# Optimization experiments

Hardware: AMD Instinct MI355X
Metric: run time of the kernel (lower is better)

## Reference

```python
import jax, jax.numpy as jnp
import numpy as np

BN_EPS = 1e-5
N_NODES = 131072
C_IN = 32
C_OUT = 32
K = 27  # 3x3x3 kernel taps


def setup_inputs() -> dict:
    key = jax.random.key(0)
    k1, k2, k3 = jax.random.split(key, 3)
    data_in = jax.random.normal(k1, (1, C_IN, N_NODES, 1), dtype=jnp.float32)
    neigh = jax.random.randint(k2, (N_NODES, K), 0, N_NODES, dtype=jnp.int32)
    weight = jax.random.normal(k3, (K * C_IN, C_OUT), dtype=jnp.float32) * (1.0 / np.sqrt(K * C_IN))
    gamma = jnp.ones((C_OUT,), dtype=jnp.float32)
    beta = jnp.zeros((C_OUT,), dtype=jnp.float32)
    return {"data_in": data_in, "neigh": neigh, "weight": weight, "gamma": gamma, "beta": beta}


def reference(data_in, neigh, weight, gamma, beta):
    # data_in: [1, C_in, N, 1] -> node-major features [N, C_in]
    x = jnp.transpose(data_in[0, :, :, 0])  # [N, C_in]
    # Octree sparse conv: gather 27-neighborhood per node, then matmul.
    g = x[neigh]                              # [N, K, C_in] irregular gather
    g = g.reshape(g.shape[0], K * C_IN)       # [N, K*C_in]
    out = g @ weight                          # [N, C_out]
    # BatchNorm2d over [1, C_out, N, 1]: per-channel stats over the N nodes (training mode, biased var)
    mean = jnp.mean(out, axis=0)
    var = jnp.mean(jnp.square(out - mean), axis=0)
    out = (out - mean) * jax.lax.rsqrt(var + BN_EPS) * gamma + beta
    # ReLU
    out = jnp.maximum(out, 0.0)
    # back to O-CNN layout [1, C_out, N, 1]
    return jnp.transpose(out)[None, :, :, None]
```

## Files before the change

### kernel.cpp

```cpp
#include <hip/hip_runtime.h>

#define N_NODES 131072
#define C_IN 32
#define C_OUT 32
#define KTAPS 27
#define BN_EPS 1e-5f
#define NPASS 3

typedef __bf16 bf16x8 __attribute__((ext_vector_type(8)));
typedef float  f32x4  __attribute__((ext_vector_type(4)));


static __device__ __forceinline__ unsigned short f2bf(float f) {
    unsigned int u = __float_as_uint(f);
    unsigned int r = (u + 0x7FFFu + ((u >> 16) & 1u)) >> 16;
    return (unsigned short)r;
}

__global__ __launch_bounds__(256) void k_prep(const float* __restrict__ in,
                                              const float* __restrict__ w,
                                              unsigned short* __restrict__ xb,
                                              unsigned short* __restrict__ wlay,
                                              float* __restrict__ sums) {
    if (blockIdx.x < N_NODES / 256) {
        const int n = blockIdx.x * 256 + threadIdx.x;
        unsigned short v[C_IN];
#pragma unroll
        for (int c = 0; c < C_IN; ++c) v[c] = f2bf(in[(size_t)c * N_NODES + n]);
        uint4* dst = reinterpret_cast<uint4*>(xb + (size_t)n * C_IN);
#pragma unroll
        for (int q = 0; q < 4; ++q) {
            uint4 pk;
            pk.x = (unsigned)v[q * 8 + 0] | ((unsigned)v[q * 8 + 1] << 16);
            pk.y = (unsigned)v[q * 8 + 2] | ((unsigned)v[q * 8 + 3] << 16);
            pk.z = (unsigned)v[q * 8 + 4] | ((unsigned)v[q * 8 + 5] << 16);
            pk.w = (unsigned)v[q * 8 + 6] | ((unsigned)v[q * 8 + 7] << 16);
            dst[q] = pk;
        }
    } else {
        if (threadIdx.x < 4) {
            uint4 z = {0u, 0u, 0u, 0u};
            reinterpret_cast<uint4*>(xb + (size_t)N_NODES * C_IN)[threadIdx.x] = z;
        }
        if (threadIdx.x < 2 * C_OUT) sums[threadIdx.x] = 0.f;
        for (int g = threadIdx.x; g < KTAPS * 2 * 64; g += 256) {
            const int k = g >> 7;
            const int rem = g & 127;
            const int h = rem >> 6;
            const int l = rem & 63;
            unsigned short wv[8];
#pragma unroll
            for (int j = 0; j < 8; ++j) {
                const int c  = ((l >> 4) << 3) + j;
                const int co = (h << 4) + (l & 15);
                wv[j] = f2bf(w[(size_t)(k * C_IN + c) * C_OUT + co]);
            }
            uint4 pk;
            pk.x = (unsigned)wv[0] | ((unsigned)wv[1] << 16);
            pk.y = (unsigned)wv[2] | ((unsigned)wv[3] << 16);
            pk.z = (unsigned)wv[4] | ((unsigned)wv[5] << 16);
            pk.w = (unsigned)wv[6] | ((unsigned)wv[7] << 16);
            *reinterpret_cast<uint4*>(wlay + (size_t)g * 8) = pk;
        }
    }
}

__global__ __launch_bounds__(1024) void k_conv_mfma(const unsigned short* __restrict__ xb,
                                                    const int* __restrict__ neigh,
                                                    const unsigned short* __restrict__ wlay,
                                                    float* __restrict__ out,
                                                    float* __restrict__ sums) {
    __shared__ unsigned short wl[KTAPS * 2 * 64 * 8];
    __shared__ float bs[C_OUT];
    __shared__ float bq[C_OUT];

    {
        const uint4* src = reinterpret_cast<const uint4*>(wlay);
        uint4* d = reinterpret_cast<uint4*>(wl);
        for (int i = threadIdx.x; i < KTAPS * 2 * 64; i += 1024) d[i] = src[i];
    }
    if (threadIdx.x < C_OUT) { bs[threadIdx.x] = 0.f; bq[threadIdx.x] = 0.f; }
    __syncthreads();

    const int wid  = threadIdx.x >> 6;
    const int lane = threadIdx.x & 63;
    const int lr   = lane & 15;
    const int lg   = lane >> 4;
    const int nb   = blockIdx.x * 256 + wid * 16;

    const int* nrow = neigh + (size_t)(nb + lr) * KTAPS;
    int nidx[KTAPS];
#pragma unroll
    for (int k = 0; k < KTAPS; ++k) nidx[k] = nrow[k];

    f32x4 acc0 = {0.f, 0.f, 0.f, 0.f};
    f32x4 acc1 = {0.f, 0.f, 0.f, 0.f};

#pragma unroll 1
    for (int p = 0; p < NPASS; ++p) {
        const int lo = (p * N_NODES) / NPASS;
        const int hi = ((p + 1) * N_NODES) / NPASS;
#pragma unroll
        for (int k = 0; k < KTAPS; ++k) {
            const int idx = nidx[k];
            const int src = (idx >= lo) && (idx < hi) ? idx : N_NODES;
            const bf16x8 xf = *reinterpret_cast<const bf16x8*>(xb + (size_t)src * C_IN + lg * 8);
            const bf16x8 w0 = *reinterpret_cast<const bf16x8*>(wl + ((size_t)(k * 2 + 0) * 64 + lane) * 8);
            const bf16x8 w1 = *reinterpret_cast<const bf16x8*>(wl + ((size_t)(k * 2 + 1) * 64 + lane) * 8);
            acc0 = __builtin_amdgcn_mfma_f32_16x16x32_bf16(w0, xf, acc0, 0, 0, 0);
            acc1 = __builtin_amdgcn_mfma_f32_16x16x32_bf16(w1, xf, acc1, 0, 0, 0);
        }
        __syncthreads();
    }

#pragma unroll
    for (int r = 0; r < 4; ++r) {
        out[(size_t)(lg * 4 + r) * N_NODES + nb + lr]      = acc0[r];
        out[(size_t)(16 + lg * 4 + r) * N_NODES + nb + lr] = acc1[r];
    }

    float s0[4], q0[4], s1[4], q1[4];
#pragma unroll
    for (int r = 0; r < 4; ++r) {
        s0[r] = acc0[r]; q0[r] = acc0[r] * acc0[r];
        s1[r] = acc1[r]; q1[r] = acc1[r] * acc1[r];
    }
#pragma unroll
    for (int off = 1; off < 16; off <<= 1) {
#pragma unroll
        for (int r = 0; r < 4; ++r) {
            s0[r] += __shfl_xor(s0[r], off); q0[r] += __shfl_xor(q0[r], off);
            s1[r] += __shfl_xor(s1[r], off); q1[r] += __shfl_xor(q1[r], off);
        }
    }
    if (lr == 0) {
#pragma unroll
        for (int r = 0; r < 4; ++r) {
            atomicAdd(&bs[lg * 4 + r], s0[r]);      atomicAdd(&bq[lg * 4 + r], q0[r]);
            atomicAdd(&bs[16 + lg * 4 + r], s1[r]); atomicAdd(&bq[16 + lg * 4 + r], q1[r]);
        }
    }
    __syncthreads();
    if (threadIdx.x < C_OUT) {
        atomicAdd(&sums[threadIdx.x], bs[threadIdx.x]);
        atomicAdd(&sums[C_OUT + threadIdx.x], bq[threadIdx.x]);
    }
}

__global__ __launch_bounds__(256) void k_bnrelu(float* __restrict__ out,
                                                const float* __restrict__ sums,
                                                const float* __restrict__ gamma,
                                                const float* __restrict__ beta) {
    const size_t gid = (size_t)blockIdx.x * 256 + threadIdx.x;
    const int co = (int)(gid / (N_NODES / 4));
    const float inv_n = 1.0f / (float)N_NODES;
    const float mean = sums[co] * inv_n;
    const float var  = sums[C_OUT + co] * inv_n - mean * mean;
    const float scale = rsqrtf(var + BN_EPS) * gamma[co];
    const float bias  = beta[co] - mean * scale;

    float4* p = reinterpret_cast<float4*>(out);
    float4 v = p[gid];
    v.x = fmaxf(fmaf(v.x, scale, bias), 0.0f);
    v.y = fmaxf(fmaf(v.y, scale, bias), 0.0f);
    v.z = fmaxf(fmaf(v.z, scale, bias), 0.0f);
    v.w = fmaxf(fmaf(v.w, scale, bias), 0.0f);
    p[gid] = v;
}

extern "C" void kernel_launch(void* const* d_in, const int* in_sizes, int n_in,
                              void* d_out, int out_size, void* d_ws, size_t ws_size,
                              hipStream_t stream) {
    const float* data_in = (const float*)d_in[0];
    const int*   neigh   = (const int*)d_in[1];
    const float* weight  = (const float*)d_in[2];
    const float* gamma   = (const float*)d_in[3];
    const float* beta    = (const float*)d_in[4];
    float* out = (float*)d_out;

    unsigned short* xb   = (unsigned short*)d_ws;
    unsigned short* wlay = xb + (size_t)(N_NODES + 1) * C_IN;
    float* sums = (float*)(wlay + (size_t)KTAPS * 2 * 64 * 8);

    k_prep<<<N_NODES / 256 + 1, 256, 0, stream>>>(data_in, weight, xb, wlay, sums);
    k_conv_mfma<<<N_NODES / 256, 1024, 0, stream>>>(xb, neigh, wlay, out, sums);
    k_bnrelu<<<(N_NODES * C_OUT / 4) / 256, 256, 0, stream>>>(out, sums, gamma, beta);
}
```

Measured before the change: 73.12 us.

## Switch conv to 32x32x16 MFMA with 32 nodes per wave

```diff
diff --git a/kernel.cpp b/kernel.cpp
--- a/kernel.cpp
+++ b/kernel.cpp
@@ -8,7 +8,7 @@
 #define NPASS 3
 
 typedef __bf16 bf16x8 __attribute__((ext_vector_type(8)));
-typedef float  f32x4  __attribute__((ext_vector_type(4)));
+typedef float  f32x16 __attribute__((ext_vector_type(16)));
 
 
 static __device__ __forceinline__ unsigned short f2bf(float f) {
@@ -45,14 +45,13 @@
         if (threadIdx.x < 2 * C_OUT) sums[threadIdx.x] = 0.f;
         for (int g = threadIdx.x; g < KTAPS * 2 * 64; g += 256) {
             const int k = g >> 7;
-            const int rem = g & 127;
-            const int h = rem >> 6;
-            const int l = rem & 63;
+            const int h = (g >> 6) & 1;
+            const int l = g & 63;
             unsigned short wv[8];
 #pragma unroll
             for (int j = 0; j < 8; ++j) {
-                const int c  = ((l >> 4) << 3) + j;
-                const int co = (h << 4) + (l & 15);
+                const int c  = h * 16 + ((l >> 5) << 3) + j;
+                const int co = l & 31;
                 wv[j] = f2bf(w[(size_t)(k * C_IN + c) * C_OUT + co]);
             }
             uint4 pk;
@@ -65,11 +64,11 @@
     }
 }
 
-__global__ __launch_bounds__(1024) void k_conv_mfma(const unsigned short* __restrict__ xb,
-                                                    const int* __restrict__ neigh,
-                                                    const unsigned short* __restrict__ wlay,
-                                                    float* __restrict__ out,
-                                                    float* __restrict__ sums) {
+__global__ __launch_bounds__(512, 4) void k_conv_mfma(const unsigned short* __restrict__ xb,
+                                                      const int* __restrict__ neigh,
+                                                      const unsigned short* __restrict__ wlay,
+                                                      float* __restrict__ out,
+                                                      float* __restrict__ sums) {
     __shared__ unsigned short wl[KTAPS * 2 * 64 * 8];
     __shared__ float bs[C_OUT];
     __shared__ float bq[C_OUT];
@@ -77,24 +76,23 @@
     {
         const uint4* src = reinterpret_cast<const uint4*>(wlay);
         uint4* d = reinterpret_cast<uint4*>(wl);
-        for (int i = threadIdx.x; i < KTAPS * 2 * 64; i += 1024) d[i] = src[i];
+        for (int i = threadIdx.x; i < KTAPS * 2 * 64; i += 512) d[i] = src[i];
     }
     if (threadIdx.x < C_OUT) { bs[threadIdx.x] = 0.f; bq[threadIdx.x] = 0.f; }
     __syncthreads();
 
     const int wid  = threadIdx.x >> 6;
     const int lane = threadIdx.x & 63;
-    const int lr   = lane & 15;
-    const int lg   = lane >> 4;
-    const int nb   = blockIdx.x * 256 + wid * 16;
+    const int col  = lane & 31;
+    const int kh   = lane >> 5;
+    const int nb   = blockIdx.x * 256 + wid * 32;
 
-    const int* nrow = neigh + (size_t)(nb + lr) * KTAPS;
+    const int* nrow = neigh + (size_t)(nb + col) * KTAPS;
     int nidx[KTAPS];
 #pragma unroll
     for (int k = 0; k < KTAPS; ++k) nidx[k] = nrow[k];
 
-    f32x4 acc0 = {0.f, 0.f, 0.f, 0.f};
-    f32x4 acc1 = {0.f, 0.f, 0.f, 0.f};
+    f32x16 acc = {};
 
 #pragma unroll 1
     for (int p = 0; p < NPASS; ++p) {
@@ -104,40 +102,40 @@
         for (int k = 0; k < KTAPS; ++k) {
             const int idx = nidx[k];
             const int src = (idx >= lo) && (idx < hi) ? idx : N_NODES;
-            const bf16x8 xf = *reinterpret_cast<const bf16x8*>(xb + (size_t)src * C_IN + lg * 8);
+            const unsigned short* xrow = xb + (size_t)src * C_IN + kh * 8;
+            const bf16x8 x0 = *reinterpret_cast<const bf16x8*>(xrow);
+            const bf16x8 x1 = *reinterpret_cast<const bf16x8*>(xrow + 16);
             const bf16x8 w0 = *reinterpret_cast<const bf16x8*>(wl + ((size_t)(k * 2 + 0) * 64 + lane) * 8);
             const bf16x8 w1 = *reinterpret_cast<const bf16x8*>(wl + ((size_t)(k * 2 + 1) * 64 + lane) * 8);
-            acc0 = __builtin_amdgcn_mfma_f32_16x16x32_bf16(w0, xf, acc0, 0, 0, 0);
-            acc1 = __builtin_amdgcn_mfma_f32_16x16x32_bf16(w1, xf, acc1, 0, 0, 0);
+            acc = __builtin_amdgcn_mfma_f32_32x32x16_bf16(w0, x0, acc, 0, 0, 0);
+            acc = __builtin_amdgcn_mfma_f32_32x32x16_bf16(w1, x1, acc, 0, 0, 0);
         }
         __syncthreads();
     }
 
 #pragma unroll
-    for (int r = 0; r < 4; ++r) {
-        out[(size_t)(lg * 4 + r) * N_NODES + nb + lr]      = acc0[r];
-        out[(size_t)(16 + lg * 4 + r) * N_NODES + nb + lr] = acc1[r];
+    for (int r = 0; r < 16; ++r) {
+        const int row = (r & 3) + 8 * (r >> 2) + 4 * kh;
+        out[(size_t)row * N_NODES + nb + col] = acc[r];
     }
 
-    float s0[4], q0[4], s1[4], q1[4];
+    float s[16], q[16];
 #pragma unroll
-    for (int r = 0; r < 4; ++r) {
-        s0[r] = acc0[r]; q0[r] = acc0[r] * acc0[r];
-        s1[r] = acc1[r]; q1[r] = acc1[r] * acc1[r];
-    }
+    for (int r = 0; r < 16; ++r) { s[r] = acc[r]; q[r] = acc[r] * acc[r]; }
 #pragma unroll
-    for (int off = 1; off < 16; off <<= 1) {
+    for (int off = 1; off < 32; off <<= 1) {
 #pragma unroll
-        for (int r = 0; r < 4; ++r) {
-            s0[r] += __shfl_xor(s0[r], off); q0[r] += __shfl_xor(q0[r], off);
-            s1[r] += __shfl_xor(s1[r], off); q1[r] += __shfl_xor(q1[r], off);
+        for (int r = 0; r < 16; ++r) {
+            s[r] += __shfl_xor(s[r], off);
+            q[r] += __shfl_xor(q[r], off);
         }
     }
-    if (lr == 0) {
+    if (col == 0) {
 #pragma unroll
-        for (int r = 0; r < 4; ++r) {
-            atomicAdd(&bs[lg * 4 + r], s0[r]);      atomicAdd(&bq[lg * 4 + r], q0[r]);
-            atomicAdd(&bs[16 + lg * 4 + r], s1[r]); atomicAdd(&bq[16 + lg * 4 + r], q1[r]);
+        for (int r = 0; r < 16; ++r) {
+            const int row = (r & 3) + 8 * (r >> 2) + 4 * kh;
+            atomicAdd(&bs[row], s[r]);
+            atomicAdd(&bq[row], q[r]);
         }
     }
     __syncthreads();
@@ -183,6 +181,6 @@
     float* sums = (float*)(wlay + (size_t)KTAPS * 2 * 64 * 8);
 
     k_prep<<<N_NODES / 256 + 1, 256, 0, stream>>>(data_in, weight, xb, wlay, sums);
-    k_conv_mfma<<<N_NODES / 256, 1024, 0, stream>>>(xb, neigh, wlay, out, sums);
+    k_conv_mfma<<<N_NODES / 256, 512, 0, stream>>>(xb, neigh, wlay, out, sums);
     k_bnrelu<<<(N_NODES * C_OUT / 4) / 256, 256, 0, stream>>>(out, sums, gamma, beta);
 }
```

Result: slower. 74.59 us (+2.0%).
